# Performance work log

Measured on AMD Instinct MI355X. Metric: run time of the kernel, lower is better.

## Reference

```python
import jax, jax.numpy as jnp
import numpy as np

N, E = 50000, 800000
IN, HID, OUT, H = 128, 16, 16, 4


def setup_inputs() -> dict:
    key = jax.random.key(0)
    ks = jax.random.split(key, 11)
    sc = 0.1
    return {
        "features": jax.random.normal(ks[0], (N, IN), jnp.float32),
        "src": jax.random.randint(ks[1], (E,), 0, N, dtype=jnp.int64) if jax.config.jax_enable_x64 else jax.random.randint(ks[1], (E,), 0, N).astype(jnp.int32),
        "dst": jax.random.randint(ks[2], (E,), 0, N).astype(jnp.int32),
        "W1": jax.random.normal(ks[3], (H * HID, IN), jnp.float32) * sc,
        "al1": jax.random.normal(ks[4], (H, HID), jnp.float32) * sc,
        "ar1": jax.random.normal(ks[5], (H, HID), jnp.float32) * sc,
        "b1": jax.random.normal(ks[6], (H * HID,), jnp.float32) * sc,
        "W2": jax.random.normal(ks[7], (H * OUT, H * HID), jnp.float32) * sc,
        "al2": jax.random.normal(ks[8], (H, OUT), jnp.float32) * sc,
        "ar2": jax.random.normal(ks[9], (H, OUT), jnp.float32) * sc,
        "b2": jax.random.normal(ks[10], (H * OUT,), jnp.float32) * sc,
    }


def gat_conv(src, dst, feat, W, al, ar, b, heads, dout):
    """DGL-style GATConv: fc -> edge attention -> dst-softmax -> scatter-sum."""
    n = feat.shape[0]
    h = (feat @ W.T).reshape(n, heads, dout)            # [N,H,D]
    el = jnp.einsum("nhd,hd->nh", h, al)                # [N,H]
    er = jnp.einsum("nhd,hd->nh", h, ar)                # [N,H]
    e = jax.nn.leaky_relu(el[src] + er[dst], 0.2)       # [E,H]
    m = jax.ops.segment_max(e, dst, num_segments=n)     # per-dst max, [N,H]
    a = jnp.exp(e - m[dst])                             # [E,H]
    s = jax.ops.segment_sum(a, dst, num_segments=n)     # [N,H]
    alpha = a / s[dst]                                  # edge softmax, [E,H]
    out = jax.ops.segment_sum(alpha[:, :, None] * h[src], dst, num_segments=n)
    return out + b.reshape(1, heads, dout)              # [N,H,D]


def reference(features, src, dst, W1, al1, ar1, b1, W2, al2, ar2, b2):
    h = gat_conv(src, dst, features, W1, al1, ar1, b1, H, HID).reshape(N, H * HID)
    h = jax.nn.relu(h)
    h = gat_conv(src, dst, h, W2, al2, ar2, b2, H, OUT).mean(axis=1)  # mean over heads
    return jax.nn.log_softmax(h, axis=1)
```

## Files before the change

### kernel.cpp

```cpp
#include <hip/hip_runtime.h>
#include <math.h>

#define N_NODES 50000
#define N_EDGES 800000
#define NPART 8
#define PART_SZ ((N_NODES + NPART - 1) / NPART)
#define CAP 64
#define SCAT_BLOCKS 4096
#define FC_BLOCKS 784

typedef __attribute__((ext_vector_type(8))) short short8;
typedef __attribute__((ext_vector_type(8))) unsigned short ushort8;
typedef __attribute__((ext_vector_type(4))) float v4f;
typedef __attribute__((ext_vector_type(2))) float v2f;
typedef __attribute__((ext_vector_type(4))) int int4v;

__device__ __forceinline__ float bf2f(unsigned short h) {
    return __uint_as_float(((unsigned int)h) << 16);
}
__device__ __forceinline__ unsigned short f2bf(float f) {
    unsigned int u = __float_as_uint(f);
    u += 0x7fff + ((u >> 16) & 1);
    return (unsigned short)(u >> 16);
}

__device__ __forceinline__ short8 load_afrag(const float* X, size_t row, int K,
                                             int kc, int quad) {
    const float* p = X + row * K + kc * 32 + quad * 8;
    const float4 t0 = *(const float4*)p;
    const float4 t1 = *(const float4*)(p + 4);
    short8 a;
    a[0] = (short)f2bf(t0.x); a[1] = (short)f2bf(t0.y);
    a[2] = (short)f2bf(t0.z); a[3] = (short)f2bf(t0.w);
    a[4] = (short)f2bf(t1.x); a[5] = (short)f2bf(t1.y);
    a[6] = (short)f2bf(t1.z); a[7] = (short)f2bf(t1.w);
    return a;
}
__device__ __forceinline__ short8 load_afrag(const unsigned short* X, size_t row,
                                             int K, int kc, int quad) {
    return *(const short8*)(X + row * K + kc * 32 + quad * 8);
}

template <int K, typename XT>
__device__ __forceinline__ void fc_att_body(
    const XT* __restrict__ X, const float* __restrict__ W,
    const float* __restrict__ al, const float* __restrict__ ar,
    unsigned short* __restrict__ Hout, float* __restrict__ el,
    float* __restrict__ er, int nTiles, int blk, unsigned short* Wlds)
{
    constexpr int KP = K + 8;
    constexpr int NKC = K / 32;
    const int tid = threadIdx.x;
    for (int i = tid; i < 64 * K; i += 256) {
        const int r = i / K, c = i - r * K;
        Wlds[r * KP + c] = f2bf(W[i]);
    }
    __syncthreads();

    const int lane = tid & 63;
    const int wave = tid >> 6;
    const int d = lane & 15;
    const int quad = lane >> 4;

    const int tile = blk * 4 + wave;
    if (tile >= nTiles) return;
    const int node0 = tile * 16;

    short8 wf[4][NKC];
#pragma unroll
    for (int ng = 0; ng < 4; ++ng) {
#pragma unroll
        for (int kc = 0; kc < NKC; ++kc) {
            wf[ng][kc] = *(const short8*)&Wlds[(ng * 16 + d) * KP + kc * 32 + quad * 8];
        }
    }

    v4f cc[4] = {{0.f,0.f,0.f,0.f},{0.f,0.f,0.f,0.f},{0.f,0.f,0.f,0.f},{0.f,0.f,0.f,0.f}};
#pragma unroll
    for (int kc = 0; kc < NKC; ++kc) {
        const short8 a = load_afrag(X, (size_t)(node0 + d), K, kc, quad);
        cc[0] = __builtin_amdgcn_mfma_f32_16x16x32_bf16(a, wf[0][kc], cc[0], 0, 0, 0);
        cc[1] = __builtin_amdgcn_mfma_f32_16x16x32_bf16(a, wf[1][kc], cc[1], 0, 0, 0);
        cc[2] = __builtin_amdgcn_mfma_f32_16x16x32_bf16(a, wf[2][kc], cc[2], 0, 0, 0);
        cc[3] = __builtin_amdgcn_mfma_f32_16x16x32_bf16(a, wf[3][kc], cc[3], 0, 0, 0);
    }

#pragma unroll
    for (int ng = 0; ng < 4; ++ng) {
        const float alv = al[ng * 16 + d];
        const float arv = ar[ng * 16 + d];
        const v4f c = cc[ng];
#pragma unroll
        for (int r = 0; r < 4; ++r) {
            const int node = node0 + quad * 4 + r;
            Hout[(size_t)node * 64 + ng * 16 + d] = f2bf(c[r]);
            float vel = c[r] * alv;
            float ver = c[r] * arv;
#pragma unroll
            for (int off = 1; off < 16; off <<= 1) {
                vel += __shfl_xor(vel, off);
                ver += __shfl_xor(ver, off);
            }
            if (d == 0) {
                el[node * 4 + ng] = vel;
                er[node * 4 + ng] = ver;
            }
        }
    }
}

template <int K, typename XT>
__global__ __launch_bounds__(256) void fc_att_mfma(
    const XT* __restrict__ X, const float* __restrict__ W,
    const float* __restrict__ al, const float* __restrict__ ar,
    unsigned short* __restrict__ Hout, float* __restrict__ el,
    float* __restrict__ er, int nTiles)
{
    __shared__ __align__(16) unsigned short Wlds[64 * (K + 8)];
    fc_att_body<K, XT>(X, W, al, ar, Hout, el, er, nTiles, (int)blockIdx.x, Wlds);
}

__global__ __launch_bounds__(256) void l1_fused_kernel(
    const float* __restrict__ X, const float* __restrict__ W,
    const float* __restrict__ al, const float* __restrict__ ar,
    unsigned short* __restrict__ Hout, float* __restrict__ el,
    float* __restrict__ er,
    const int* __restrict__ src, const int* __restrict__ dst,
    int* __restrict__ cnt16, unsigned short* __restrict__ col)
{
    __shared__ __align__(16) unsigned short Wlds[64 * (128 + 8)];
    if ((int)blockIdx.x < FC_BLOCKS) {
        fc_att_body<128, float>(X, W, al, ar, Hout, el, er,
                                N_NODES / 16, (int)blockIdx.x, Wlds);
    } else {
        const int bid = (int)blockIdx.x - FC_BLOCKS;
        const int part = bid & (NPART - 1);
        const int lo = part * PART_SZ;
        const int hi = lo + PART_SZ;
        const int tid_p = (bid >> 3) * 256 + (int)threadIdx.x;
        const int stride = (SCAT_BLOCKS / NPART) * 256;
        const int4v* dst4 = (const int4v*)dst;
        const int4v* src4 = (const int4v*)src;
        const int NQ = N_EDGES / 4;
        for (int q = tid_p; q < NQ; q += 2 * stride) {
            const int q2 = q + stride;
            const bool ok2 = q2 < NQ;
            const int4v dA = __builtin_nontemporal_load(dst4 + q);
            const int4v sA = __builtin_nontemporal_load(src4 + q);
            const int4v dB = ok2 ? __builtin_nontemporal_load(dst4 + q2) : (int4v){-1,-1,-1,-1};
            const int4v sB = ok2 ? __builtin_nontemporal_load(src4 + q2) : (int4v){0,0,0,0};
            const int dd[8] = {dA[0], dA[1], dA[2], dA[3], dB[0], dB[1], dB[2], dB[3]};
            const int ss[8] = {sA[0], sA[1], sA[2], sA[3], sB[0], sB[1], sB[2], sB[3]};
            int pos[8];
#pragma unroll
            for (int j = 0; j < 8; ++j) {
                pos[j] = -1;
                if (dd[j] >= lo && dd[j] < hi)
                    pos[j] = atomicAdd(&cnt16[(unsigned)dd[j] * 16], 1);
            }
#pragma unroll
            for (int j = 0; j < 8; ++j) {
                if (pos[j] >= 0 && pos[j] < CAP)
                    col[(unsigned)dd[j] * CAP + pos[j]] = (unsigned short)ss[j];
            }
        }
    }
}

__device__ __forceinline__ void agg_walk_pair(
    const unsigned short* __restrict__ colrow, int len, int len_max,
    const float* __restrict__ el, const unsigned int* __restrict__ Hf32,
    int hb, int hl, float erv_a,
    float& accL_out, float& accH_out, float& sacc_a_out)
{
    const int j_a = hl >> 2;
    const unsigned h_a = (unsigned)(hl & 3);
    const int hd = hl >> 3;
    float accL0 = 0.f, accL1 = 0.f, accH0 = 0.f, accH1 = 0.f;
    float sacc_a = 0.f;
    for (int i = 0; i < len_max; i += 16) {
        const ushort8 sv0 = __builtin_nontemporal_load((const ushort8*)(colrow + i));
        const ushort8 sv1 = __builtin_nontemporal_load((const ushort8*)(colrow + i + 8));
        const int rm = len - i;
        const unsigned sa0 = (unsigned)colrow[i + j_a];
        const unsigned sa1 = (unsigned)colrow[i + 8 + j_a];
        float x0 = el[sa0 * 4u + h_a] + erv_a;
        float x1 = el[sa1 * 4u + h_a] + erv_a;
        x0 = fmaxf(x0, 0.2f * x0);
        x1 = fmaxf(x1, 0.2f * x1);
        float a0 = __expf(x0);
        float a1 = __expf(x1);
        a0 = (j_a < rm) ? a0 : 0.f;
        a1 = (j_a + 8 < rm) ? a1 : 0.f;
        sacc_a += a0 + a1;
        unsigned uu[16];
#pragma unroll
        for (int j = 0; j < 8; ++j)
            uu[j] = Hf32[(unsigned)sv0[j] * 32u + (unsigned)hl];
#pragma unroll
        for (int j = 0; j < 8; ++j)
            uu[8 + j] = Hf32[(unsigned)sv1[j] * 32u + (unsigned)hl];
#pragma unroll
        for (int j = 0; j < 8; ++j) {
            const float aj = __shfl(a0, hb + j * 4 + hd);
            const float lo = __uint_as_float(uu[j] << 16);
            const float hi = __uint_as_float(uu[j] & 0xffff0000u);
            if (j & 1) { accL1 = fmaf(aj, lo, accL1); accH1 = fmaf(aj, hi, accH1); }
            else       { accL0 = fmaf(aj, lo, accL0); accH0 = fmaf(aj, hi, accH0); }
        }
#pragma unroll
        for (int j = 0; j < 8; ++j) {
            const float aj = __shfl(a1, hb + j * 4 + hd);
            const float lo = __uint_as_float(uu[8 + j] << 16);
            const float hi = __uint_as_float(uu[8 + j] & 0xffff0000u);
            if (j & 1) { accL1 = fmaf(aj, lo, accL1); accH1 = fmaf(aj, hi, accH1); }
            else       { accL0 = fmaf(aj, lo, accL0); accH0 = fmaf(aj, hi, accH0); }
        }
    }
    sacc_a += __shfl_xor(sacc_a, 4);
    sacc_a += __shfl_xor(sacc_a, 8);
    sacc_a += __shfl_xor(sacc_a, 16);
    sacc_a_out = sacc_a;
    accL_out = accL0 + accL1;
    accH_out = accH0 + accH1;
}

__global__ __launch_bounds__(256) void agg_relu_kernel(
    const int* __restrict__ cnt16, const unsigned short* __restrict__ col,
    const float* __restrict__ el, const float* __restrict__ er,
    const unsigned int* __restrict__ Hf32, const float* __restrict__ b,
    unsigned int* __restrict__ out32, int n)
{
    const int lane = threadIdx.x & 63;
    const int wave = threadIdx.x >> 6;
    const int hl = lane & 31;
    const int hb = lane & 32;
    const int node = blockIdx.x * 8 + wave * 2 + (lane >> 5);
    if (node >= n) return;
    const int hd = hl >> 3;
    const int cg = hd * 16 + (hl & 7) * 2;
    const float erv_a = er[node * 4 + (hl & 3)];
    const int len = min(cnt16[(unsigned)node * 16], CAP);
    const int len_max = max(len, __shfl_xor(len, 32));
    float accL, accH, sacc_a;
    agg_walk_pair(col + (unsigned)node * CAP, len, len_max, el, Hf32,
                  hb, hl, erv_a, accL, accH, sacc_a);
    const float sc = __shfl(sacc_a, hb + hd);
    float vL = sc > 0.f ? accL / sc : 0.f;
    float vH = sc > 0.f ? accH / sc : 0.f;
    vL += b[cg];   vH += b[cg + 1];
    vL = vL > 0.f ? vL : 0.f;
    vH = vH > 0.f ? vH : 0.f;
    const unsigned u = (unsigned)f2bf(vL) | ((unsigned)f2bf(vH) << 16);
    __builtin_nontemporal_store(u, out32 + (size_t)node * 32 + hl);
}

__global__ __launch_bounds__(256) void agg_final_kernel(
    const int* __restrict__ cnt16, const unsigned short* __restrict__ col,
    const float* __restrict__ el, const float* __restrict__ er,
    const unsigned int* __restrict__ Hf32, const float* __restrict__ b,
    float* __restrict__ out, int n)
{
    const int lane = threadIdx.x & 63;
    const int wave = threadIdx.x >> 6;
    const int hl = lane & 31;
    const int hb = lane & 32;
    const int node = blockIdx.x * 8 + wave * 2 + (lane >> 5);
    if (node >= n) return;
    const int hd = hl >> 3;
    const int cg = hd * 16 + (hl & 7) * 2;
    const float erv_a = er[node * 4 + (hl & 3)];
    const int len = min(cnt16[(unsigned)node * 16], CAP);
    const int len_max = max(len, __shfl_xor(len, 32));
    float accL, accH, sacc_a;
    agg_walk_pair(col + (unsigned)node * CAP, len, len_max, el, Hf32,
                  hb, hl, erv_a, accL, accH, sacc_a);
    const float sc = __shfl(sacc_a, hb + hd);
    float zL = sc > 0.f ? accL / sc : 0.f;
    float zH = sc > 0.f ? accH / sc : 0.f;
    zL += b[cg];   zH += b[cg + 1];
    zL += __shfl_xor(zL, 8);  zL += __shfl_xor(zL, 16);  zL *= 0.25f;
    zH += __shfl_xor(zH, 8);  zH += __shfl_xor(zH, 16);  zH *= 0.25f;
    float m = fmaxf(zL, zH);
    m = fmaxf(m, __shfl_xor(m, 1));
    m = fmaxf(m, __shfl_xor(m, 2));
    m = fmaxf(m, __shfl_xor(m, 4));
    float se = __expf(zL - m) + __expf(zH - m);
    se += __shfl_xor(se, 1);
    se += __shfl_xor(se, 2);
    se += __shfl_xor(se, 4);
    const float lse = __logf(se);
    if (hl < 8) {
        v2f r;
        r[0] = zL - m - lse;
        r[1] = zH - m - lse;
        __builtin_nontemporal_store(r, (v2f*)(out + (size_t)node * 16 + hl * 2));
    }
}

extern "C" void kernel_launch(void* const* d_in, const int* in_sizes, int n_in,
                              void* d_out, int out_size, void* d_ws, size_t ws_size,
                              hipStream_t stream)
{
    const float* feat = (const float*)d_in[0];
    const int*   src  = (const int*)d_in[1];
    const int*   dst  = (const int*)d_in[2];
    const float* W1   = (const float*)d_in[3];
    const float* al1  = (const float*)d_in[4];
    const float* ar1  = (const float*)d_in[5];
    const float* b1   = (const float*)d_in[6];
    const float* W2   = (const float*)d_in[7];
    const float* al2  = (const float*)d_in[8];
    const float* ar2  = (const float*)d_in[9];
    const float* b2   = (const float*)d_in[10];
    float* out = (float*)d_out;

    float* el  = (float*)d_ws;
    float* er  = el + N_NODES * 4;
    int*   cnt16 = (int*)(er + N_NODES * 4);
    uintptr_t p = ((uintptr_t)(cnt16 + N_NODES * 16) + 15) & ~(uintptr_t)15;
    unsigned short* col = (unsigned short*)p;
    unsigned short* A   = col + (size_t)N_NODES * CAP + 64;
    unsigned short* B   = A + (size_t)N_NODES * 64;

    const int NT = N_NODES / 16;
    const int FB = (NT + 3) / 4;
    const int AB2 = (N_NODES + 7) / 8;

    (void)hipMemsetAsync(cnt16, 0, (size_t)((char*)A - (char*)cnt16), stream);

    l1_fused_kernel<<<FC_BLOCKS + SCAT_BLOCKS, 256, 0, stream>>>(
        feat, W1, al1, ar1, A, el, er, src, dst, cnt16, col);
    agg_relu_kernel<<<AB2, 256, 0, stream>>>(cnt16, col, el, er,
                                             (const unsigned int*)A, b1,
                                             (unsigned int*)B, N_NODES);

    fc_att_mfma<64, unsigned short><<<FB, 256, 0, stream>>>(B, W2, al2, ar2, A, el, er, NT);
    agg_final_kernel<<<AB2, 256, 0, stream>>>(cnt16, col, el, er,
                                              (const unsigned int*)A, b2, out, N_NODES);
}
```

Measured before the change: 183.7 us.

## Fuse layer-1 aggregation with layer-2 FC/attention in one kernel

Merges the layer-1 aggregation+ReLU kernel with the layer-2 MFMA projection and attention-logit kernel. Each 512-thread block aggregates 16 nodes, keeps the ReLU output in LDS, and runs a 16x64x64 bf16 MFMA to produce H2, el2 and er2. This removes the global round trip of the hidden activations and one launch. It also stores el2/er2 interleaved inside the padded cnt16 slots (stride 16) to reuse workspace. The cost is an extra W2 conversion into LDS per block and half the waves idling after the sync.

```diff
diff --git a/kernel.cpp b/kernel.cpp
--- a/kernel.cpp
+++ b/kernel.cpp
@@ -15,9 +15,6 @@
 typedef __attribute__((ext_vector_type(2))) float v2f;
 typedef __attribute__((ext_vector_type(4))) int int4v;
 
-__device__ __forceinline__ float bf2f(unsigned short h) {
-    return __uint_as_float(((unsigned int)h) << 16);
-}
 __device__ __forceinline__ unsigned short f2bf(float f) {
     unsigned int u = __float_as_uint(f);
     u += 0x7fff + ((u >> 16) & 1);
@@ -36,10 +33,6 @@
     a[6] = (short)f2bf(t1.z); a[7] = (short)f2bf(t1.w);
     return a;
 }
-__device__ __forceinline__ short8 load_afrag(const unsigned short* X, size_t row,
-                                             int K, int kc, int quad) {
-    return *(const short8*)(X + row * K + kc * 32 + quad * 8);
-}
 
 template <int K, typename XT>
 __device__ __forceinline__ void fc_att_body(
@@ -107,17 +100,6 @@
             }
         }
     }
-}
-
-template <int K, typename XT>
-__global__ __launch_bounds__(256) void fc_att_mfma(
-    const XT* __restrict__ X, const float* __restrict__ W,
-    const float* __restrict__ al, const float* __restrict__ ar,
-    unsigned short* __restrict__ Hout, float* __restrict__ el,
-    float* __restrict__ er, int nTiles)
-{
-    __shared__ __align__(16) unsigned short Wlds[64 * (K + 8)];
-    fc_att_body<K, XT>(X, W, al, ar, Hout, el, er, nTiles, (int)blockIdx.x, Wlds);
 }
 
 __global__ __launch_bounds__(256) void l1_fused_kernel(
@@ -167,6 +149,52 @@
     }
 }
 
+template <int ELS>
+__device__ __forceinline__ void agg_iter16(
+    const unsigned short* __restrict__ colrow, int i, int rm,
+    const float* __restrict__ el, const unsigned int* __restrict__ Hf32,
+    int hb, int hl, int j_a, unsigned h_a, int hd, float erv_a,
+    float& accL0, float& accL1, float& accH0, float& accH1, float& sacc_a)
+{
+    const ushort8 sv0 = __builtin_nontemporal_load((const ushort8*)(colrow + i));
+    const ushort8 sv1 = __builtin_nontemporal_load((const ushort8*)(colrow + i + 8));
+    const unsigned sa0 = (unsigned)colrow[i + j_a];
+    const unsigned sa1 = (unsigned)colrow[i + 8 + j_a];
+    float x0 = el[sa0 * ELS + h_a] + erv_a;
+    float x1 = el[sa1 * ELS + h_a] + erv_a;
+    x0 = fmaxf(x0, 0.2f * x0);
+    x1 = fmaxf(x1, 0.2f * x1);
+    float a0 = __expf(x0);
+    float a1 = __expf(x1);
+    a0 = (j_a < rm) ? a0 : 0.f;
+    a1 = (j_a + 8 < rm) ? a1 : 0.f;
+    sacc_a += a0 + a1;
+    unsigned uu[16];
+#pragma unroll
+    for (int j = 0; j < 8; ++j)
+        uu[j] = Hf32[(unsigned)sv0[j] * 32u + (unsigned)hl];
+#pragma unroll
+    for (int j = 0; j < 8; ++j)
+        uu[8 + j] = Hf32[(unsigned)sv1[j] * 32u + (unsigned)hl];
+#pragma unroll
+    for (int j = 0; j < 8; ++j) {
+        const float aj = __shfl(a0, hb + j * 4 + hd);
+        const float lo = __uint_as_float(uu[j] << 16);
+        const float hi = __uint_as_float(uu[j] & 0xffff0000u);
+        if (j & 1) { accL1 = fmaf(aj, lo, accL1); accH1 = fmaf(aj, hi, accH1); }
+        else       { accL0 = fmaf(aj, lo, accL0); accH0 = fmaf(aj, hi, accH0); }
+    }
+#pragma unroll
+    for (int j = 0; j < 8; ++j) {
+        const float aj = __shfl(a1, hb + j * 4 + hd);
+        const float lo = __uint_as_float(uu[8 + j] << 16);
+        const float hi = __uint_as_float(uu[8 + j] & 0xffff0000u);
+        if (j & 1) { accL1 = fmaf(aj, lo, accL1); accH1 = fmaf(aj, hi, accH1); }
+        else       { accL0 = fmaf(aj, lo, accL0); accH0 = fmaf(aj, hi, accH0); }
+    }
+}
+
+template <int ELS>
 __device__ __forceinline__ void agg_walk_pair(
     const unsigned short* __restrict__ colrow, int len, int len_max,
     const float* __restrict__ el, const unsigned int* __restrict__ Hf32,
@@ -178,45 +206,11 @@
     const int hd = hl >> 3;
     float accL0 = 0.f, accL1 = 0.f, accH0 = 0.f, accH1 = 0.f;
     float sacc_a = 0.f;
-    for (int i = 0; i < len_max; i += 16) {
-        const ushort8 sv0 = __builtin_nontemporal_load((const ushort8*)(colrow + i));
-        const ushort8 sv1 = __builtin_nontemporal_load((const ushort8*)(colrow + i + 8));
-        const int rm = len - i;
-        const unsigned sa0 = (unsigned)colrow[i + j_a];
-        const unsigned sa1 = (unsigned)colrow[i + 8 + j_a];
-        float x0 = el[sa0 * 4u + h_a] + erv_a;
-        float x1 = el[sa1 * 4u + h_a] + erv_a;
-        x0 = fmaxf(x0, 0.2f * x0);
-        x1 = fmaxf(x1, 0.2f * x1);
-        float a0 = __expf(x0);
-        float a1 = __expf(x1);
-        a0 = (j_a < rm) ? a0 : 0.f;
-        a1 = (j_a + 8 < rm) ? a1 : 0.f;
-        sacc_a += a0 + a1;
-        unsigned uu[16];
-#pragma unroll
-        for (int j = 0; j < 8; ++j)
-            uu[j] = Hf32[(unsigned)sv0[j] * 32u + (unsigned)hl];
-#pragma unroll
-        for (int j = 0; j < 8; ++j)
-            uu[8 + j] = Hf32[(unsigned)sv1[j] * 32u + (unsigned)hl];
-#pragma unroll
-        for (int j = 0; j < 8; ++j) {
-            const float aj = __shfl(a0, hb + j * 4 + hd);
-            const float lo = __uint_as_float(uu[j] << 16);
-            const float hi = __uint_as_float(uu[j] & 0xffff0000u);
-            if (j & 1) { accL1 = fmaf(aj, lo, accL1); accH1 = fmaf(aj, hi, accH1); }
-            else       { accL0 = fmaf(aj, lo, accL0); accH0 = fmaf(aj, hi, accH0); }
-        }
-#pragma unroll
-        for (int j = 0; j < 8; ++j) {
-            const float aj = __shfl(a1, hb + j * 4 + hd);
-            const float lo = __uint_as_float(uu[8 + j] << 16);
-            const float hi = __uint_as_float(uu[8 + j] & 0xffff0000u);
-            if (j & 1) { accL1 = fmaf(aj, lo, accL1); accH1 = fmaf(aj, hi, accH1); }
-            else       { accL0 = fmaf(aj, lo, accL0); accH0 = fmaf(aj, hi, accH0); }
-        }
-    }
+    agg_iter16<ELS>(colrow, 0, len, el, Hf32, hb, hl, j_a, h_a, hd, erv_a,
+                    accL0, accL1, accH0, accH1, sacc_a);
+    for (int i = 16; i < len_max; i += 16)
+        agg_iter16<ELS>(colrow, i, len - i, el, Hf32, hb, hl, j_a, h_a, hd,
+                        erv_a, accL0, accL1, accH0, accH1, sacc_a);
     sacc_a += __shfl_xor(sacc_a, 4);
     sacc_a += __shfl_xor(sacc_a, 8);
     sacc_a += __shfl_xor(sacc_a, 16);
@@ -225,11 +219,89 @@
     accH_out = accH0 + accH1;
 }
 
-__global__ __launch_bounds__(256) void agg_relu_kernel(
+__global__ __launch_bounds__(512) void agg1_fc2_fused(
     const int* __restrict__ cnt16, const unsigned short* __restrict__ col,
-    const float* __restrict__ el, const float* __restrict__ er,
+    const float* __restrict__ el1, const float* __restrict__ er1,
+    const unsigned int* __restrict__ H1, const float* __restrict__ b1,
+    const float* __restrict__ W2, const float* __restrict__ al2,
+    const float* __restrict__ ar2,
+    unsigned short* __restrict__ H2,
+    float* __restrict__ el2, float* __restrict__ er2)
+{
+    __shared__ __align__(16) unsigned short W2lds[64 * 72];
+    __shared__ __align__(16) unsigned int Hlds[16 * 33];
+
+    const int tid = threadIdx.x;
+    const int lane = tid & 63;
+    const int wave = tid >> 6;
+    const int hl = lane & 31;
+    const int hb = lane & 32;
+    const int nl = wave * 2 + (lane >> 5);
+    const int node = (int)blockIdx.x * 16 + nl;
+    const int hd = hl >> 3;
+    const int cg = hd * 16 + (hl & 7) * 2;
+
+    const int len = min(cnt16[(unsigned)node * 16], CAP);
+    const float erv_a = er1[node * 4 + (hl & 3)];
+    const float bL = b1[cg];
+    const float bH = b1[cg + 1];
+
+    for (int i = tid; i < 64 * 64; i += 512) {
+        const int r = i >> 6, c = i & 63;
+        W2lds[r * 72 + c] = f2bf(W2[i]);
+    }
+
+    const int len_max = max(len, __shfl_xor(len, 32));
+    float accL, accH, sacc_a;
+    agg_walk_pair<4>(col + (unsigned)node * CAP, len, len_max, el1, H1,
+                     hb, hl, erv_a, accL, accH, sacc_a);
+    const float sc = __shfl(sacc_a, hb + hd);
+    float vL = sc > 0.f ? accL / sc : 0.f;
+    float vH = sc > 0.f ? accH / sc : 0.f;
+    vL += bL;  vH += bH;
+    vL = vL > 0.f ? vL : 0.f;
+    vH = vH > 0.f ? vH : 0.f;
+    Hlds[nl * 33 + hl] = (unsigned)f2bf(vL) | ((unsigned)f2bf(vH) << 16);
+    __syncthreads();
+    if (wave >= 4) return;
+
+    const int ng = wave;
+    const int d = lane & 15;
+    const int quad = lane >> 4;
+    const unsigned short* lds16 = (const unsigned short*)Hlds;
+    const short8 wf0 = *(const short8*)&W2lds[(ng * 16 + d) * 72 + quad * 8];
+    const short8 wf1 = *(const short8*)&W2lds[(ng * 16 + d) * 72 + 32 + quad * 8];
+    const short8 a0 = *(const short8*)&lds16[(unsigned)d * 66 + quad * 8];
+    const short8 a1 = *(const short8*)&lds16[(unsigned)d * 66 + 32 + quad * 8];
+    v4f c0 = {0.f, 0.f, 0.f, 0.f};
+    c0 = __builtin_amdgcn_mfma_f32_16x16x32_bf16(a0, wf0, c0, 0, 0, 0);
+    c0 = __builtin_amdgcn_mfma_f32_16x16x32_bf16(a1, wf1, c0, 0, 0, 0);
+
+    const float alv = al2[ng * 16 + d];
+    const float arv = ar2[ng * 16 + d];
+#pragma unroll
+    for (int r = 0; r < 4; ++r) {
+        const int node2 = (int)blockIdx.x * 16 + quad * 4 + r;
+        H2[(size_t)node2 * 64 + ng * 16 + d] = f2bf(c0[r]);
+        float vel = c0[r] * alv;
+        float ver = c0[r] * arv;
+#pragma unroll
+        for (int off = 1; off < 16; off <<= 1) {
+            vel += __shfl_xor(vel, off);
+            ver += __shfl_xor(ver, off);
+        }
+        if (d == 0) {
+            el2[node2 * 16 + ng] = vel;
+            er2[node2 * 16 + ng] = ver;
+        }
+    }
+}
+
+__global__ __launch_bounds__(256) void agg_final_kernel(
+    const int* __restrict__ cnt16, const unsigned short* __restrict__ col,
+    const float* __restrict__ el2, const float* __restrict__ er2,
     const unsigned int* __restrict__ Hf32, const float* __restrict__ b,
-    unsigned int* __restrict__ out32, int n)
+    float* __restrict__ out, int n)
 {
     const int lane = threadIdx.x & 63;
     const int wave = threadIdx.x >> 6;
@@ -239,46 +311,18 @@
     if (node >= n) return;
     const int hd = hl >> 3;
     const int cg = hd * 16 + (hl & 7) * 2;
-    const float erv_a = er[node * 4 + (hl & 3)];
+    const float erv_a = er2[node * 16 + (hl & 3)];
+    const float bL = b[cg];
+    const float bH = b[cg + 1];
     const int len = min(cnt16[(unsigned)node * 16], CAP);
     const int len_max = max(len, __shfl_xor(len, 32));
     float accL, accH, sacc_a;
-    agg_walk_pair(col + (unsigned)node * CAP, len, len_max, el, Hf32,
-                  hb, hl, erv_a, accL, accH, sacc_a);
-    const float sc = __shfl(sacc_a, hb + hd);
-    float vL = sc > 0.f ? accL / sc : 0.f;
-    float vH = sc > 0.f ? accH / sc : 0.f;
-    vL += b[cg];   vH += b[cg + 1];
-    vL = vL > 0.f ? vL : 0.f;
-    vH = vH > 0.f ? vH : 0.f;
-    const unsigned u = (unsigned)f2bf(vL) | ((unsigned)f2bf(vH) << 16);
-    __builtin_nontemporal_store(u, out32 + (size_t)node * 32 + hl);
-}
-
-__global__ __launch_bounds__(256) void agg_final_kernel(
-    const int* __restrict__ cnt16, const unsigned short* __restrict__ col,
-    const float* __restrict__ el, const float* __restrict__ er,
-    const unsigned int* __restrict__ Hf32, const float* __restrict__ b,
-    float* __restrict__ out, int n)
-{
-    const int lane = threadIdx.x & 63;
-    const int wave = threadIdx.x >> 6;
-    const int hl = lane & 31;
-    const int hb = lane & 32;
-    const int node = blockIdx.x * 8 + wave * 2 + (lane >> 5);
-    if (node >= n) return;
-    const int hd = hl >> 3;
-    const int cg = hd * 16 + (hl & 7) * 2;
-    const float erv_a = er[node * 4 + (hl & 3)];
-    const int len = min(cnt16[(unsigned)node * 16], CAP);
-    const int len_max = max(len, __shfl_xor(len, 32));
-    float accL, accH, sacc_a;
-    agg_walk_pair(col + (unsigned)node * CAP, len, len_max, el, Hf32,
-                  hb, hl, erv_a, accL, accH, sacc_a);
+    agg_walk_pair<16>(col + (unsigned)node * CAP, len, len_max, el2, Hf32,
+                      hb, hl, erv_a, accL, accH, sacc_a);
     const float sc = __shfl(sacc_a, hb + hd);
     float zL = sc > 0.f ? accL / sc : 0.f;
     float zH = sc > 0.f ? accH / sc : 0.f;
-    zL += b[cg];   zH += b[cg + 1];
+    zL += bL;   zH += bH;
     zL += __shfl_xor(zL, 8);  zL += __shfl_xor(zL, 16);  zL *= 0.25f;
     zH += __shfl_xor(zH, 8);  zH += __shfl_xor(zH, 16);  zH *= 0.25f;
     float m = fmaxf(zL, zH);
@@ -315,27 +359,29 @@
     const float* b2   = (const float*)d_in[10];
     float* out = (float*)d_out;
 
-    float* el  = (float*)d_ws;
-    float* er  = el + N_NODES * 4;
-    int*   cnt16 = (int*)(er + N_NODES * 4);
+    float* el1 = (float*)d_ws;
+    float* er1 = el1 + N_NODES * 4;
+    int*   cnt16 = (int*)(er1 + N_NODES * 4);
     uintptr_t p = ((uintptr_t)(cnt16 + N_NODES * 16) + 15) & ~(uintptr_t)15;
     unsigned short* col = (unsigned short*)p;
     unsigned short* A   = col + (size_t)N_NODES * CAP + 64;
     unsigned short* B   = A + (size_t)N_NODES * 64;
-
-    const int NT = N_NODES / 16;
-    const int FB = (NT + 3) / 4;
+    float* el2 = (float*)cnt16 + 4;
+    float* er2 = (float*)cnt16 + 8;
+
     const int AB2 = (N_NODES + 7) / 8;
+    const int TILES = N_NODES / 16;
 
     (void)hipMemsetAsync(cnt16, 0, (size_t)((char*)A - (char*)cnt16), stream);
 
     l1_fused_kernel<<<FC_BLOCKS + SCAT_BLOCKS, 256, 0, stream>>>(
-        feat, W1, al1, ar1, A, el, er, src, dst, cnt16, col);
-    agg_relu_kernel<<<AB2, 256, 0, stream>>>(cnt16, col, el, er,
-                                             (const unsigned int*)A, b1,
-                                             (unsigned int*)B, N_NODES);
-
-    fc_att_mfma<64, unsigned short><<<FB, 256, 0, stream>>>(B, W2, al2, ar2, A, el, er, NT);
-    agg_final_kernel<<<AB2, 256, 0, stream>>>(cnt16, col, el, er,
-                                              (const unsigned int*)A, b2, out, N_NODES);
-}
+        feat, W1, al1, ar1, A, el1, er1, src, dst, cnt16, col);
+
+    agg1_fc2_fused<<<TILES, 512, 0, stream>>>(
+        cnt16, col, el1, er1, (const unsigned int*)A, b1,
+        W2, al2, ar2, B, el2, er2);
+
+    agg_final_kernel<<<AB2, 256, 0, stream>>>(cnt16, col, el2, er2,
+                                              (const unsigned int*)B, b2,
+                                              out, N_NODES);
+}
```

New measurement: 179.6 us. 2.2% less time.
